# Optimization experiments

Measured on AMD Instinct MI355X. Metric: run time of the kernel, lower is better.

The kernel has to match this reference:

```python
import jax, jax.numpy as jnp
import numpy as np

N_CAPS, R, CIN, COUT = 10, 1152, 8, 16  # digit caps, primary caps (32*6*6), caps dims
B = 256


def setup_inputs() -> dict:
    key = jax.random.key(0)
    k1, k2 = jax.random.split(key)
    x = jax.random.normal(k1, (B, R, CIN), dtype=jnp.float32)
    # learned transform W: [num_capsules, num_route_nodes, in_channels, out_channels]
    W = jax.random.normal(k2, (N_CAPS, R, CIN, COUT), dtype=jnp.float32)
    return {"x": x, "W": W}


def squash(t, axis=-1):
    sq = jnp.sum(t * t, axis=axis, keepdims=True)
    return sq / (1.0 + sq) * t / jnp.sqrt(sq)


def reference(x, W):
    # u_hat = (x[None,:,:,None,:] @ W[:,None]) -> [N_CAPS, B, R, 1, COUT]; squeeze the 1.
    u_hat = jnp.einsum('bri,nrio->nbro', x, W)  # [N, B, R, O]
    # NOTE: the original forward returns v_j INSIDE the routing loop, so exactly one
    # iteration executes: b_ij = 0 => c_ij = softmax(zeros, dim=route) = 1/R (uniform).
    c = 1.0 / u_hat.shape[2]
    s = jnp.sum(c * u_hat, axis=2, keepdims=True)  # [N, B, 1, O]
    v = squash(s, axis=-1)
    return v[:, :, :, None, :]  # [N, B, 1, 1, O] to match torch v_j shape
```

## Files before the change

### kernel.cpp

```cpp
#include <hip/hip_runtime.h>

#define RNODES 1152
#define KDIM 9216
#define COUT 16
#define NCAPS 10
#define WSTRIDE (KDIM*COUT)

#define LROW 40
#define WBUF (NCAPS*COUT*LROW)
#define STEPS 9
#define SPLITS 32
#define NBLK 512
#define MT 16
#define PARTL (MT*COUT*NCAPS)
#define PARTL4 (PARTL/4)

using bf16x8 = __attribute__((ext_vector_type(8))) short;
using f32x4  = __attribute__((ext_vector_type(4))) float;

__device__ __forceinline__ unsigned short f2bf(float f) {
  unsigned int u = __builtin_bit_cast(unsigned int, f);
  return (unsigned short)((u + 0x8000u) >> 16);
}

__global__ __launch_bounds__(256, 2) void caps_gemm(const float* __restrict__ x,
                                                    const float* __restrict__ W,
                                                    float* __restrict__ ws) {
  __shared__ unsigned short wbuf[2][WBUF];
  const int tid = threadIdx.x;
  const int bid = blockIdx.x;
  const int mt  = bid >> 5;
  const int ks  = bid & 31;
  const int b0  = mt * MT;
  const int k0  = ks * (STEPS * 32);

  const int lane = tid & 63;
  const int wv   = tid >> 6;
  const int q    = lane >> 4;
  const int m16  = lane & 15;

  int u_n[5], u_kl[5], u_of[5];
#pragma unroll
  for (int j = 0; j < 5; ++j) {
    const int u  = j * 256 + tid;
    u_n[j]  = u >> 7;
    const int rem = u & 127;
    u_kl[j] = rem >> 2;
    u_of[j] = (rem & 3) << 2;
  }

  const float* xrow = x + (size_t)(b0 + m16) * KDIM + k0 + q * 8;

  float4 pw[3][5];
  float4 pa[3][2];

  auto load_step = [&](int s, int slot) {
#pragma unroll
    for (int j = 0; j < 5; ++j)
      pw[slot][j] = *(const float4*)(W + (size_t)u_n[j] * WSTRIDE +
                                     (size_t)(k0 + s * 32 + u_kl[j]) * COUT + u_of[j]);
    pa[slot][0] = *(const float4*)(xrow + s * 32);
    pa[slot][1] = *(const float4*)(xrow + s * 32 + 4);
  };

  load_step(0, 0);
  load_step(1, 1);
  load_step(2, 2);

  f32x4 acc[3];
#pragma unroll
  for (int i = 0; i < 3; ++i) acc[i] = (f32x4){0.f, 0.f, 0.f, 0.f};

  const int qrot = (q + (m16 & 3) + (m16 >> 2)) & 3;
  int rdoff[3];
#pragma unroll
  for (int j = 0; j < 3; ++j) {
    const int nt  = wv * 3 + j;
    const int nt2 = (nt < NCAPS) ? nt : 0;
    rdoff[j] = (nt2 * COUT + m16) * LROW + (qrot << 3);
  }

#pragma unroll
  for (int s = 0; s < STEPS; ++s) {
    const int slot = s % 3;
    unsigned short* b = &wbuf[s & 1][0];
#pragma unroll
    for (int j = 0; j < 5; ++j) {
      const int kl  = u_kl[j];
      const int klo = kl & 7, kblk = kl >> 3;
      const float* v = (const float*)&pw[slot][j];
#pragma unroll
      for (int r = 0; r < 4; ++r) {
        const int c   = u_n[j] * COUT + u_of[j] + r;
        const int pos = klo | (((kblk + (c & 3) + ((c >> 2) & 3)) & 3) << 3);
        b[c * LROW + pos] = f2bf(v[r]);
      }
    }
    __syncthreads();

    bf16x8 a;
    a[0] = (short)f2bf(pa[slot][0].x); a[1] = (short)f2bf(pa[slot][0].y);
    a[2] = (short)f2bf(pa[slot][0].z); a[3] = (short)f2bf(pa[slot][0].w);
    a[4] = (short)f2bf(pa[slot][1].x); a[5] = (short)f2bf(pa[slot][1].y);
    a[6] = (short)f2bf(pa[slot][1].z); a[7] = (short)f2bf(pa[slot][1].w);

    if (s + 3 < STEPS) load_step(s + 3, slot);

#pragma unroll
    for (int j = 0; j < 3; ++j) {
      bf16x8 bf = *(const bf16x8*)&b[rdoff[j]];
      acc[j] = __builtin_amdgcn_mfma_f32_16x16x32_bf16(a, bf, acc[j], 0, 0, 0);
    }
  }

  float* P = ws + (size_t)bid * PARTL;
  const int prow = q * 4;
#pragma unroll
  for (int j = 0; j < 3; ++j) {
    const int nt = wv * 3 + j;
    if (nt < NCAPS) {
#pragma unroll
      for (int r = 0; r < 4; ++r)
        P[nt * (MT * COUT) + (prow + r) * COUT + m16] = acc[j][r];
    }
  }
}

__global__ __launch_bounds__(128, 1) void caps_reduce(const float* __restrict__ ws,
                                                      float* __restrict__ out) {
  const int f  = blockIdx.x * 128 + threadIdx.x;
  const int n  = f >> 10;
  const int b  = (f >> 2) & 255;
  const int o4 = f & 3;
  const int mt = b >> 4, row = b & 15;

  const float4* base = (const float4*)ws + (size_t)(mt * SPLITS) * PARTL4
                       + n * (MT * COUT / 4) + row * 4 + o4;
  float4 s0 = {0,0,0,0}, s1 = {0,0,0,0}, s2 = {0,0,0,0}, s3 = {0,0,0,0};
#pragma unroll
  for (int kk = 0; kk < SPLITS; kk += 4) {
    float4 a0 = base[(size_t)(kk + 0) * PARTL4];
    float4 a1 = base[(size_t)(kk + 1) * PARTL4];
    float4 a2 = base[(size_t)(kk + 2) * PARTL4];
    float4 a3 = base[(size_t)(kk + 3) * PARTL4];
    s0.x += a0.x; s0.y += a0.y; s0.z += a0.z; s0.w += a0.w;
    s1.x += a1.x; s1.y += a1.y; s1.z += a1.z; s1.w += a1.w;
    s2.x += a2.x; s2.y += a2.y; s2.z += a2.z; s2.w += a2.w;
    s3.x += a3.x; s3.y += a3.y; s3.z += a3.z; s3.w += a3.w;
  }
  const float inv = 1.0f / (float)RNODES;
  float4 s;
  s.x = ((s0.x + s1.x) + (s2.x + s3.x)) * inv;
  s.y = ((s0.y + s1.y) + (s2.y + s3.y)) * inv;
  s.z = ((s0.z + s1.z) + (s2.z + s3.z)) * inv;
  s.w = ((s0.w + s1.w) + (s2.w + s3.w)) * inv;

  float sq = s.x * s.x + s.y * s.y + s.z * s.z + s.w * s.w;
  sq += __shfl_xor(sq, 1);
  sq += __shfl_xor(sq, 2);
  const float g = sqrtf(sq) / (1.0f + sq);
  s.x *= g; s.y *= g; s.z *= g; s.w *= g;

  ((float4*)out)[f] = s;
}

extern "C" void kernel_launch(void* const* d_in, const int* in_sizes, int n_in,
                              void* d_out, int out_size, void* d_ws, size_t ws_size,
                              hipStream_t stream) {
  const float* x = (const float*)d_in[0];
  const float* W = (const float*)d_in[1];
  float* ws  = (float*)d_ws;
  float* out = (float*)d_out;

  caps_gemm<<<dim3(NBLK), dim3(256), 0, stream>>>(x, W, ws);
  caps_reduce<<<dim3(80), dim3(128), 0, stream>>>(ws, out);
}
```

Baseline: 73.69 us.

## Pre-convert inputs to bf16 fragment layout and drop LDS staging in GEMM

Adds a conversion kernel that writes x and W as bf16 into workspace, already arranged in the per-lane MFMA fragment order. The GEMM kernel then loads operand fragments directly from global memory in a simple two-stage register pipeline, with no shared memory and no barriers. This removes in-loop conversion, LDS writes and synchronization, at the cost of an extra launch and extra global write/read traffic for the bf16 copies.

```diff
diff --git a/kernel.cpp b/kernel.cpp
--- a/kernel.cpp
+++ b/kernel.cpp
@@ -6,14 +6,17 @@
 #define NCAPS 10
 #define WSTRIDE (KDIM*COUT)
 
-#define LROW 40
-#define WBUF (NCAPS*COUT*LROW)
+#define SPLITS 32
 #define STEPS 9
-#define SPLITS 32
-#define NBLK 512
 #define MT 16
+#define GBLK 512
 #define PARTL (MT*COUT*NCAPS)
 #define PARTL4 (PARTL/4)
+
+#define XAB_UNITS (16*1152*16)
+#define WT_OFF   ((size_t)XAB_UNITS*16)
+#define WT_UNITS (NCAPS*1152*16)
+#define PART_OFF (WT_OFF + (size_t)WT_UNITS*16)
 
 using bf16x8 = __attribute__((ext_vector_type(8))) short;
 using f32x4  = __attribute__((ext_vector_type(4))) float;
@@ -23,105 +26,103 @@
   return (unsigned short)((u + 0x8000u) >> 16);
 }
 
-__global__ __launch_bounds__(256, 2) void caps_gemm(const float* __restrict__ x,
+__device__ __forceinline__ void pack_store8(unsigned short* dst, const float* v) {
+  union { unsigned short us[8]; uint4 q; } t;
+#pragma unroll
+  for (int i = 0; i < 8; ++i) t.us[i] = f2bf(v[i]);
+  *(uint4*)dst = t.q;
+}
+
+__global__ __launch_bounds__(256) void caps_convert(const float* __restrict__ x,
                                                     const float* __restrict__ W,
-                                                    float* __restrict__ ws) {
-  __shared__ unsigned short wbuf[2][WBUF];
-  const int tid = threadIdx.x;
-  const int bid = blockIdx.x;
-  const int mt  = bid >> 5;
-  const int ks  = bid & 31;
-  const int b0  = mt * MT;
-  const int k0  = ks * (STEPS * 32);
+                                                    unsigned short* __restrict__ wsb) {
+  const int bx = blockIdx.x, tid = threadIdx.x;
+  if (bx < 1152) {
+    const int bt = bx / 72;
+    const int r  = (bx % 72) * 256 + tid;
+    const int kb = r >> 4, br = r & 15;
+    const float* src = x + (size_t)(bt * 16 + br) * KDIM + kb * 8;
+    float4 v0 = *(const float4*)src;
+    float4 v1 = *(const float4*)(src + 4);
+    float v[8] = {v0.x, v0.y, v0.z, v0.w, v1.x, v1.y, v1.z, v1.w};
+    pack_store8(wsb + ((size_t)bt * 18432 + r) * 8, v);
+  } else {
+    const int b2 = bx - 1152;
+    const int n  = b2 / 72;
+    const int r  = (b2 % 72) * 256 + tid;
+    const int kb = r >> 4, o = r & 15;
+    const float* src = W + (size_t)n * WSTRIDE + (size_t)kb * 128 + o;
+    float v[8];
+#pragma unroll
+    for (int j = 0; j < 8; ++j) v[j] = src[j * 16];
+    pack_store8(wsb + (WT_OFF / 2) + ((size_t)n * 18432 + r) * 8, v);
+  }
+}
 
+__global__ __launch_bounds__(256, 2) void caps_gemm(const unsigned short* __restrict__ xab,
+                                                    const unsigned short* __restrict__ wt,
+                                                    float* __restrict__ part) {
+  const int tid  = threadIdx.x, bid = blockIdx.x;
+  const int mt   = bid >> 5;
+  const int ks   = bid & 31;
   const int lane = tid & 63;
   const int wv   = tid >> 6;
   const int q    = lane >> 4;
   const int m16  = lane & 15;
+  const int kb0  = ks * (STEPS * 4);
 
-  int u_n[5], u_kl[5], u_of[5];
+  const unsigned short* ap = xab + ((size_t)(mt * 1152 + kb0 + q) * 16 + m16) * 8;
+  const unsigned short* bp0, *bp1, *bp2;
+  int nt[3];
 #pragma unroll
-  for (int j = 0; j < 5; ++j) {
-    const int u  = j * 256 + tid;
-    u_n[j]  = u >> 7;
-    const int rem = u & 127;
-    u_kl[j] = rem >> 2;
-    u_of[j] = (rem & 3) << 2;
+  for (int j = 0; j < 3; ++j) nt[j] = wv * 3 + j;
+  {
+    const int n0 = nt[0] < NCAPS ? nt[0] : 0;
+    const int n1 = nt[1] < NCAPS ? nt[1] : 0;
+    const int n2 = nt[2] < NCAPS ? nt[2] : 0;
+    bp0 = wt + ((size_t)(n0 * 1152 + kb0 + q) * 16 + m16) * 8;
+    bp1 = wt + ((size_t)(n1 * 1152 + kb0 + q) * 16 + m16) * 8;
+    bp2 = wt + ((size_t)(n2 * 1152 + kb0 + q) * 16 + m16) * 8;
   }
-
-  const float* xrow = x + (size_t)(b0 + m16) * KDIM + k0 + q * 8;
-
-  float4 pw[3][5];
-  float4 pa[3][2];
-
-  auto load_step = [&](int s, int slot) {
-#pragma unroll
-    for (int j = 0; j < 5; ++j)
-      pw[slot][j] = *(const float4*)(W + (size_t)u_n[j] * WSTRIDE +
-                                     (size_t)(k0 + s * 32 + u_kl[j]) * COUT + u_of[j]);
-    pa[slot][0] = *(const float4*)(xrow + s * 32);
-    pa[slot][1] = *(const float4*)(xrow + s * 32 + 4);
-  };
-
-  load_step(0, 0);
-  load_step(1, 1);
-  load_step(2, 2);
 
   f32x4 acc[3];
 #pragma unroll
   for (int i = 0; i < 3; ++i) acc[i] = (f32x4){0.f, 0.f, 0.f, 0.f};
 
-  const int qrot = (q + (m16 & 3) + (m16 >> 2)) & 3;
-  int rdoff[3];
+  bf16x8 aA[3], aB[3], bA[3][3], bB[3][3];
+
+  auto loadg = [&](bf16x8 (&AF)[3], bf16x8 (&BF)[3][3], int g) {
+#pragma unroll
+    for (int s = 0; s < 3; ++s) {
+      const int off = (g * 3 + s) * 512;
+      AF[s]    = *(const bf16x8*)(ap  + off);
+      BF[0][s] = *(const bf16x8*)(bp0 + off);
+      BF[1][s] = *(const bf16x8*)(bp1 + off);
+      BF[2][s] = *(const bf16x8*)(bp2 + off);
+    }
+  };
+  auto mmag = [&](bf16x8 (&AF)[3], bf16x8 (&BF)[3][3]) {
+#pragma unroll
+    for (int s = 0; s < 3; ++s)
+#pragma unroll
+      for (int j = 0; j < 3; ++j)
+        acc[j] = __builtin_amdgcn_mfma_f32_16x16x32_bf16(AF[s], BF[j][s], acc[j], 0, 0, 0);
+  };
+
+  loadg(aA, bA, 0);
+  loadg(aB, bB, 1);
+  mmag(aA, bA);
+  loadg(aA, bA, 2);
+  mmag(aB, bB);
+  mmag(aA, bA);
+
+  float* P = part + (size_t)bid * PARTL;
 #pragma unroll
   for (int j = 0; j < 3; ++j) {
-    const int nt  = wv * 3 + j;
-    const int nt2 = (nt < NCAPS) ? nt : 0;
-    rdoff[j] = (nt2 * COUT + m16) * LROW + (qrot << 3);
-  }
-
-#pragma unroll
-  for (int s = 0; s < STEPS; ++s) {
-    const int slot = s % 3;
-    unsigned short* b = &wbuf[s & 1][0];
-#pragma unroll
-    for (int j = 0; j < 5; ++j) {
-      const int kl  = u_kl[j];
-      const int klo = kl & 7, kblk = kl >> 3;
-      const float* v = (const float*)&pw[slot][j];
-#pragma unroll
-      for (int r = 0; r < 4; ++r) {
-        const int c   = u_n[j] * COUT + u_of[j] + r;
-        const int pos = klo | (((kblk + (c & 3) + ((c >> 2) & 3)) & 3) << 3);
-        b[c * LROW + pos] = f2bf(v[r]);
-      }
-    }
-    __syncthreads();
-
-    bf16x8 a;
-    a[0] = (short)f2bf(pa[slot][0].x); a[1] = (short)f2bf(pa[slot][0].y);
-    a[2] = (short)f2bf(pa[slot][0].z); a[3] = (short)f2bf(pa[slot][0].w);
-    a[4] = (short)f2bf(pa[slot][1].x); a[5] = (short)f2bf(pa[slot][1].y);
-    a[6] = (short)f2bf(pa[slot][1].z); a[7] = (short)f2bf(pa[slot][1].w);
-
-    if (s + 3 < STEPS) load_step(s + 3, slot);
-
-#pragma unroll
-    for (int j = 0; j < 3; ++j) {
-      bf16x8 bf = *(const bf16x8*)&b[rdoff[j]];
-      acc[j] = __builtin_amdgcn_mfma_f32_16x16x32_bf16(a, bf, acc[j], 0, 0, 0);
-    }
-  }
-
-  float* P = ws + (size_t)bid * PARTL;
-  const int prow = q * 4;
-#pragma unroll
-  for (int j = 0; j < 3; ++j) {
-    const int nt = wv * 3 + j;
-    if (nt < NCAPS) {
+    if (nt[j] < NCAPS) {
 #pragma unroll
       for (int r = 0; r < 4; ++r)
-        P[nt * (MT * COUT) + (prow + r) * COUT + m16] = acc[j][r];
+        P[nt[j] * (MT * COUT) + (q * 4 + r) * COUT + m16] = acc[j][r];
     }
   }
 }
@@ -169,9 +170,14 @@
                               hipStream_t stream) {
   const float* x = (const float*)d_in[0];
   const float* W = (const float*)d_in[1];
-  float* ws  = (float*)d_ws;
   float* out = (float*)d_out;
 
-  caps_gemm<<<dim3(NBLK), dim3(256), 0, stream>>>(x, W, ws);
-  caps_reduce<<<dim3(80), dim3(128), 0, stream>>>(ws, out);
+  unsigned short* wsb  = (unsigned short*)d_ws;
+  const unsigned short* xab = (const unsigned short*)d_ws;
+  const unsigned short* wt  = (const unsigned short*)((const char*)d_ws + WT_OFF);
+  float* part = (float*)((char*)d_ws + PART_OFF);
+
+  caps_convert<<<dim3(1872), dim3(256), 0, stream>>>(x, W, wsb);
+  caps_gemm<<<dim3(GBLK), dim3(256), 0, stream>>>(xab, wt, part);
+  caps_reduce<<<dim3(80), dim3(128), 0, stream>>>(part, out);
 }
```

Result: slower. 75.70 us (+2.7%).
